# Optimization experiments

Hardware: AMD Instinct MI355X
Metric: run time of the kernel (lower is better)

## Reference

```python
import jax, jax.numpy as jnp
import numpy as np

VOCAB = 50257
K = 10  # accuracy_slack_size


def setup_inputs() -> dict:
    key = jax.random.key(0)
    k1, k2, k3, k4 = jax.random.split(key, 4)
    logits = jax.random.normal(k1, (4, 2048, 512), dtype=jnp.float32)
    target = jax.random.randint(k2, (4, 2048), 0, VOCAB, dtype=jnp.int64 if jax.config.jax_enable_x64 else jnp.int32)
    mask = jax.random.randint(k3, (4, 2048), 0, 2, dtype=jnp.int32)
    W = jax.random.normal(k4, (512, VOCAB), dtype=jnp.float32) * 0.02
    b = jnp.zeros((VOCAB,), dtype=jnp.float32)
    return {"logits": logits, "target": target, "mask": mask, "W": W, "b": b}


def reference(logits, target, mask, W, b):
    N = logits.shape[0] * logits.shape[1]
    x = logits.reshape(N, logits.shape[-1])            # [N, d]
    # sampled_softmax.log_prob: full log-softmax over vocab
    logp = jax.nn.log_softmax(x @ W + b, axis=-1)      # [N, V]
    _, words = jax.lax.top_k(logp, K)                  # [N, K] indices
    tgt = target.reshape(-1)                           # [N]
    msk = mask.reshape(-1).astype(jnp.float32)         # [N]
    # vectorized membership: is target among top-K predictions?
    hit = jnp.any(words == tgt[:, None], axis=1).astype(jnp.float32)
    counter = jnp.sum(hit * msk)
    all_counter = jnp.sum(msk)
    return jnp.array([counter / all_counter])
```

## Files before the change

### kernel.cpp

```cpp
#include <hip/hip_runtime.h>
#include <stdint.h>

#define V_VOCAB 50257
#define V_PAD   50304
#define NROWS   8192
#define DIM     512
#define KTOP    10
#define MARGIN  0.3f
#define ACH     8

typedef __attribute__((ext_vector_type(8))) short  short8;
typedef __attribute__((ext_vector_type(4))) float  f32x4;

struct Ctrl { int mc; int namb; int hits; int pad_; };

#define OFF_WT     0ULL
#define SZ_WT      51511296ULL
#define OFF_XC     (OFF_WT + SZ_WT)
#define SZ_XC      8388608ULL
#define OFF_BPAD   (OFF_XC + SZ_XC)
#define SZ_BPAD    (50304ULL*4)
#define OFF_ROWIDX (OFF_BPAD + SZ_BPAD)
#define OFF_THAT   (OFF_ROWIDX + 32768ULL)
#define OFF_COUNTS (OFF_THAT + 32768ULL)
#define OFF_AMB    (OFF_COUNTS + 32768ULL)
#define OFF_CTRL   (OFF_AMB + 32768ULL)
#define OFF_RK     (OFF_CTRL + 16ULL)
#define OFF_SST    (OFF_RK + 32768ULL)

#define GLOAD16(gp, lp) __builtin_amdgcn_global_load_lds( \
    (const __attribute__((address_space(1))) unsigned int*)(gp), \
    (__attribute__((address_space(3))) unsigned int*)(lp), 16, 0, 0)

__device__ __forceinline__ unsigned short f2bf(float f) {
  unsigned int u = __builtin_bit_cast(unsigned int, f);
  unsigned int r = (u + 0x7FFFu + ((u >> 16) & 1u)) >> 16;
  return (unsigned short)r;
}
__device__ __forceinline__ float bf2f(unsigned short h) {
  unsigned int u = ((unsigned int)h) << 16;
  return __builtin_bit_cast(float, u);
}

__global__ void k_prep(const int* __restrict__ mask, const float* __restrict__ b,
                       float* __restrict__ bpad, int* __restrict__ rowidx,
                       Ctrl* __restrict__ ctrl) {
  int i = blockIdx.x * 256 + threadIdx.x;
  if (i < V_PAD) bpad[i] = (i < V_VOCAB) ? b[i] : -1e30f;
  if (i < NROWS && mask[i] != 0) {
    int p = atomicAdd(&ctrl->mc, 1);
    rowidx[p] = i;
  }
}

__global__ void k_twt(const float* __restrict__ W, unsigned short* __restrict__ Wt) {
  __shared__ float lt[64][65];
  const int vbase = blockIdx.x * 64;
  const int kbase = blockIdx.y * 64;
  const int tid = threadIdx.x;
  const int krow = tid >> 6;
  const int col  = tid & 63;
  const int v    = vbase + col;
#pragma unroll
  for (int rr = 0; rr < 16; ++rr) {
    int kl = krow + rr * 4;
    float val = (v < V_VOCAB) ? W[(size_t)(kbase + kl) * V_VOCAB + v] : 0.0f;
    lt[kl][col] = val;
  }
  __syncthreads();
  const int vr = tid >> 3;
  const int kc = tid & 7;
#pragma unroll
  for (int p = 0; p < 2; ++p) {
    int vl = p * 32 + vr;
    short8 t;
#pragma unroll
    for (int j = 0; j < 8; ++j) t[j] = (short)f2bf(lt[kc * 8 + j][vl]);
    *(short8*)(Wt + (size_t)(vbase + vl) * DIM + kbase + kc * 8) = t;
  }
}

__global__ void k_xc(const float* __restrict__ x, const int* __restrict__ rowidx,
                     const Ctrl* __restrict__ ctrl, unsigned short* __restrict__ Xc) {
  const int wid = threadIdx.x >> 6, lane = threadIdx.x & 63;
  const int i = blockIdx.x * 4 + wid;
  const int mc = ctrl->mc;
  short8 t;
  if (i < mc) {
    const float* src = x + (size_t)rowidx[i] * DIM + lane * 8;
#pragma unroll
    for (int j = 0; j < 8; ++j) t[j] = (short)f2bf(src[j]);
  } else {
#pragma unroll
    for (int j = 0; j < 8; ++j) t[j] = 0;
  }
  *(short8*)(Xc + (size_t)i * DIM + lane * 8) = t;
}

__global__ void k_that(const unsigned short* __restrict__ Xc,
                       const unsigned short* __restrict__ Wt,
                       const float* __restrict__ bpad,
                       const int* __restrict__ rowidx, const int* __restrict__ target,
                       const Ctrl* __restrict__ ctrl, float* __restrict__ that) {
  const int wid = threadIdx.x >> 6, lane = threadIdx.x & 63;
  const int i = blockIdx.x * 4 + wid;
  const int mc = ctrl->mc;
  if (i >= mc) { if (lane == 0) that[i] = 1e30f; return; }
  const int tg = target[rowidx[i]];
  short8 xa = *(const short8*)(Xc + (size_t)i * DIM + lane * 8);
  short8 wa = *(const short8*)(Wt + (size_t)tg * DIM + lane * 8);
  float s = 0.f;
#pragma unroll
  for (int j = 0; j < 8; ++j)
    s += bf2f((unsigned short)xa[j]) * bf2f((unsigned short)wa[j]);
#pragma unroll
  for (int d = 1; d < 64; d <<= 1) s += __shfl_xor(s, d, 64);
  if (lane == 0) that[i] = s + bpad[tg];
}

__launch_bounds__(256, 2)
__global__ void k_count(const unsigned short* __restrict__ Xc,
                        const unsigned short* __restrict__ Wt,
                        const float* __restrict__ bpad, const float* __restrict__ that,
                        const Ctrl* __restrict__ ctrl, unsigned int* __restrict__ counts) {
  const int mc = ctrl->mc;
  const int mbase = blockIdx.y * 128;
  if (mbase >= mc) return;
  const int nbase = blockIdx.x * 128;

  __shared__ unsigned short sA[128 * 64];
  __shared__ unsigned short sB[128 * 64];
  char* sAc = (char*)sA;
  char* sBc = (char*)sB;

  const int tid = threadIdx.x;
  const int w = tid >> 6, lane = tid & 63;
  const int wm = (w >> 1) * 64, wn = (w & 1) * 64;

  const int srow = lane >> 3;
  const int s2   = (lane & 7) ^ srow;

  const char* Ab = (const char*)Xc + (size_t)mbase * 1024;
  const char* Bb = (const char*)Wt + (size_t)nbase * 1024;

  f32x4 acc[4][4];
#pragma unroll
  for (int a = 0; a < 4; ++a)
#pragma unroll
    for (int c = 0; c < 4; ++c) acc[a][c] = (f32x4)0.0f;

  for (int kt = 0; kt < 8; ++kt) {
    const int kk = kt * 128;
#pragma unroll
    for (int c = 0; c < 4; ++c) {
      const int row  = (w * 4 + c) * 8 + srow;
      const int loff = (w * 4 + c) * 1024 + lane * 16;
      GLOAD16(Ab + (size_t)row * 1024 + kk + s2 * 16, sAc + loff);
      GLOAD16(Bb + (size_t)row * 1024 + kk + s2 * 16, sBc + loff);
    }
    __syncthreads();
#pragma unroll
    for (int ks = 0; ks < 2; ++ks) {
      short8 af[4], bq[4];
#pragma unroll
      for (int mi = 0; mi < 4; ++mi) {
        const int r  = wm + mi * 16 + (lane & 15);
        const int sl = (ks * 4 + (lane >> 4)) ^ (r & 7);
        af[mi] = *(const short8*)(sAc + r * 128 + sl * 16);
      }
#pragma unroll
      for (int ni = 0; ni < 4; ++ni) {
        const int r  = wn + ni * 16 + (lane & 15);
        const int sl = (ks * 4 + (lane >> 4)) ^ (r & 7);
        bq[ni] = *(const short8*)(sBc + r * 128 + sl * 16);
      }
#pragma unroll
      for (int mi = 0; mi < 4; ++mi)
#pragma unroll
        for (int ni = 0; ni < 4; ++ni)
          acc[mi][ni] = __builtin_amdgcn_mfma_f32_16x16x32_bf16(
              af[mi], bq[ni], acc[mi][ni], 0, 0, 0);
    }
    __syncthreads();
  }

  float bv[4];
#pragma unroll
  for (int ni = 0; ni < 4; ++ni)
    bv[ni] = bpad[nbase + wn + ni * 16 + (lane & 15)];

#pragma unroll
  for (int mi = 0; mi < 4; ++mi) {
    unsigned int pc[4];
#pragma unroll
    for (int r = 0; r < 4; ++r) {
      const int m = mbase + wm + mi * 16 + (lane >> 4) * 4 + r;
      const float th  = that[m];
      const float tlo = th - MARGIN, thi = th + MARGIN;
      unsigned int p = 0;
#pragma unroll
      for (int ni = 0; ni < 4; ++ni) {
        const float s = acc[mi][ni][r] + bv[ni];
        p += (s > tlo) ? 1u : 0u;
        p += (s > thi) ? (1u << 16) : 0u;
      }
      pc[r] = p;
    }
#pragma unroll
    for (int r = 0; r < 4; ++r) {
      int p = (int)pc[r];
#pragma unroll
      for (int d = 1; d < 16; d <<= 1) p += __shfl_xor(p, d, 64);
      if ((lane & 15) == 0) {
        const int m = mbase + wm + mi * 16 + (lane >> 4) * 4 + r;
        atomicAdd(&counts[m], (unsigned int)p);
      }
    }
  }
}

__global__ void k_decide(const unsigned int* __restrict__ counts,
                         Ctrl* __restrict__ ctrl, int* __restrict__ amb) {
  const int i = blockIdx.x * 256 + threadIdx.x;
  if (i >= ctrl->mc) return;
  const unsigned int c = counts[i];
  const unsigned int lo = c & 0xFFFFu, hi = c >> 16;
  if (lo <= KTOP - 1) { atomicAdd(&ctrl->hits, 1); }
  else if (hi >= KTOP) {  }
  else { int p = atomicAdd(&ctrl->namb, 1); amb[p] = i; }
}

__global__ void k_fixt(const float* __restrict__ x, const float* __restrict__ W,
                       const float* __restrict__ b, const int* __restrict__ rowidx,
                       const int* __restrict__ target, const int* __restrict__ amb,
                       const Ctrl* __restrict__ ctrl, float* __restrict__ sst) {
  const int a = blockIdx.x * 64 + threadIdx.x;
  if (a >= ctrl->namb) return;
  const int n = rowidx[amb[a]];
  const int tg = target[n];
  float st = 0.f;
  for (int k = 0; k < DIM; ++k)
    st = fmaf(x[(size_t)n * DIM + k], W[(size_t)k * V_VOCAB + tg], st);
  sst[a] = st + b[tg];
}

__global__ void k_fixscan(const float* __restrict__ x, const float* __restrict__ W,
                          const float* __restrict__ b, const int* __restrict__ rowidx,
                          const int* __restrict__ target, const int* __restrict__ amb,
                          const float* __restrict__ sst, const Ctrl* __restrict__ ctrl,
                          int* __restrict__ rk) {
  __shared__ float sx[ACH][DIM];
  const int j = blockIdx.x * 256 + threadIdx.x;
  const int namb = ctrl->namb;
  const float bj = (j < V_VOCAB) ? b[j] : 0.f;
  for (int base = 0; base < namb; base += ACH) {
    __syncthreads();
    for (int t = threadIdx.x; t < ACH * DIM / 4; t += 256) {
      const int a  = t / (DIM / 4);
      const int kk = (t % (DIM / 4)) * 4;
      f32x4 v = (f32x4)0.f;
      if (base + a < namb) {
        const int n = rowidx[amb[base + a]];
        v = *(const f32x4*)(x + (size_t)n * DIM + kk);
      }
      *(f32x4*)(&sx[a][kk]) = v;
    }
    __syncthreads();
    if (j >= V_VOCAB) continue;
    float s[ACH];
#pragma unroll
    for (int a = 0; a < ACH; ++a) s[a] = 0.f;
    for (int k = 0; k < DIM; ++k) {
      const float wv = W[(size_t)k * V_VOCAB + j];
#pragma unroll
      for (int a = 0; a < ACH; ++a) s[a] = fmaf(sx[a][k], wv, s[a]);
    }
#pragma unroll
    for (int a = 0; a < ACH; ++a) {
      if (base + a < namb) {
        const int tg = target[rowidx[amb[base + a]]];
        const float sc = s[a] + bj;
        const float st = sst[base + a];
        if (sc > st || (sc == st && j < tg)) atomicAdd(&rk[base + a], 1);
      }
    }
  }
}

__global__ void k_fixdec(const int* __restrict__ rk, Ctrl* __restrict__ ctrl) {
  const int a = blockIdx.x * 256 + threadIdx.x;
  if (a < ctrl->namb && rk[a] <= KTOP - 1) atomicAdd(&ctrl->hits, 1);
}

__global__ void k_final(const Ctrl* __restrict__ ctrl, float* __restrict__ out) {
  out[0] = (float)ctrl->hits / (float)ctrl->mc;
}

extern "C" void kernel_launch(void* const* d_in, const int* in_sizes, int n_in,
                              void* d_out, int out_size, void* d_ws, size_t ws_size,
                              hipStream_t stream) {
  const float* x      = (const float*)d_in[0];
  const int*   target = (const int*)d_in[1];
  const int*   mask   = (const int*)d_in[2];
  const float* W      = (const float*)d_in[3];
  const float* b      = (const float*)d_in[4];
  float* out = (float*)d_out;

  char* ws = (char*)d_ws;
  unsigned short* Wt     = (unsigned short*)(ws + OFF_WT);
  unsigned short* Xc     = (unsigned short*)(ws + OFF_XC);
  float*          bpad   = (float*)(ws + OFF_BPAD);
  int*            rowidx = (int*)(ws + OFF_ROWIDX);
  float*          that   = (float*)(ws + OFF_THAT);
  unsigned int*   counts = (unsigned int*)(ws + OFF_COUNTS);
  int*            amb    = (int*)(ws + OFF_AMB);
  Ctrl*           ctrl   = (Ctrl*)(ws + OFF_CTRL);
  int*            rk     = (int*)(ws + OFF_RK);
  float*          sst    = (float*)(ws + OFF_SST);

  hipMemsetAsync(ws + OFF_COUNTS, 0, 32768 + 32768 + 16 + 32768, stream);

  k_prep   <<<197, 256, 0, stream>>>(mask, b, bpad, rowidx, ctrl);
  k_twt    <<<dim3(786, 8), 256, 0, stream>>>(W, Wt);
  k_xc     <<<2048, 256, 0, stream>>>(x, rowidx, ctrl, Xc);
  k_that   <<<2048, 256, 0, stream>>>(Xc, Wt, bpad, rowidx, target, ctrl, that);
  k_count  <<<dim3(393, 64), 256, 0, stream>>>(Xc, Wt, bpad, that, ctrl, counts);
  k_decide <<<32, 256, 0, stream>>>(counts, ctrl, amb);
  k_fixt   <<<128, 64, 0, stream>>>(x, W, b, rowidx, target, amb, ctrl, sst);
  k_fixscan<<<197, 256, 0, stream>>>(x, W, b, rowidx, target, amb, sst, ctrl, rk);
  k_fixdec <<<32, 256, 0, stream>>>(rk, ctrl);
  k_final  <<<1, 1, 0, stream>>>(ctrl, out);
}
```

Before: 544.1 us.

## Rewrite count GEMM as 256x256 tiles with double-buffered LDS pipeline

Replaces the 128x128 single-buffered k_count GEMM with a 256x256 tile using 512 threads and a 128KB double-buffered LDS ring. Global-to-LDS loads for the next K-slice are interleaved with MFMA work through explicit barriers and waitcnts, and MFMA sections run at raised priority. Workgroup IDs are remapped so consecutive blocks are spread across XCDs. Vocabulary padding grows to a multiple of 256 to fit the new tile. This adds register pressure from the 8x4 accumulators, and the large LDS footprint and hand-placed synchronisation could limit occupancy or be fragile.

Result: faster. 518.1 us (-4.8%).

```diff
diff --git a/kernel.cpp b/kernel.cpp
--- a/kernel.cpp
+++ b/kernel.cpp
@@ -2,7 +2,8 @@
 #include <stdint.h>
 
 #define V_VOCAB 50257
-#define V_PAD   50304
+#define V_PAD   50432
+#define NT_N    197
 #define NROWS   8192
 #define DIM     512
 #define KTOP    10
@@ -15,11 +16,11 @@
 struct Ctrl { int mc; int namb; int hits; int pad_; };
 
 #define OFF_WT     0ULL
-#define SZ_WT      51511296ULL
+#define SZ_WT      51642368ULL
 #define OFF_XC     (OFF_WT + SZ_WT)
 #define SZ_XC      8388608ULL
 #define OFF_BPAD   (OFF_XC + SZ_XC)
-#define SZ_BPAD    (50304ULL*4)
+#define SZ_BPAD    (50432ULL*4)
 #define OFF_ROWIDX (OFF_BPAD + SZ_BPAD)
 #define OFF_THAT   (OFF_ROWIDX + 32768ULL)
 #define OFF_COUNTS (OFF_THAT + 32768ULL)
@@ -31,6 +32,12 @@
 #define GLOAD16(gp, lp) __builtin_amdgcn_global_load_lds( \
     (const __attribute__((address_space(1))) unsigned int*)(gp), \
     (__attribute__((address_space(3))) unsigned int*)(lp), 16, 0, 0)
+
+#define SBAR()  do { asm volatile("" ::: "memory"); __builtin_amdgcn_s_barrier(); \
+                     asm volatile("" ::: "memory"); } while (0)
+#define LGKM0() asm volatile("s_waitcnt lgkmcnt(0)" ::: "memory")
+#define VM2()   asm volatile("s_waitcnt vmcnt(2)" ::: "memory")
+#define VM0()   asm volatile("s_waitcnt vmcnt(0)" ::: "memory")
 
 __device__ __forceinline__ unsigned short f2bf(float f) {
   unsigned int u = __builtin_bit_cast(unsigned int, f);
@@ -118,83 +125,126 @@
   if (lane == 0) that[i] = s + bpad[tg];
 }
 
-__launch_bounds__(256, 2)
+__launch_bounds__(512, 2)
 __global__ void k_count(const unsigned short* __restrict__ Xc,
                         const unsigned short* __restrict__ Wt,
                         const float* __restrict__ bpad, const float* __restrict__ that,
                         const Ctrl* __restrict__ ctrl, unsigned int* __restrict__ counts) {
   const int mc = ctrl->mc;
-  const int mbase = blockIdx.y * 128;
+  const int lin = blockIdx.y * NT_N + blockIdx.x;
+  const int wg  = (lin & 7) * 788 + (lin >> 3);
+  const int mt = wg & 31;
+  const int nt = wg >> 5;
+  const int mbase = mt * 256;
   if (mbase >= mc) return;
-  const int nbase = blockIdx.x * 128;
-
-  __shared__ unsigned short sA[128 * 64];
-  __shared__ unsigned short sB[128 * 64];
-  char* sAc = (char*)sA;
-  char* sBc = (char*)sB;
-
-  const int tid = threadIdx.x;
-  const int w = tid >> 6, lane = tid & 63;
-  const int wm = (w >> 1) * 64, wn = (w & 1) * 64;
-
-  const int srow = lane >> 3;
-  const int s2   = (lane & 7) ^ srow;
-
-  const char* Ab = (const char*)Xc + (size_t)mbase * 1024;
-  const char* Bb = (const char*)Wt + (size_t)nbase * 1024;
-
-  f32x4 acc[4][4];
-#pragma unroll
-  for (int a = 0; a < 4; ++a)
+  const int nbase = nt * 256;
+
+  __shared__ char lds[131072];
+
+  const int tid  = threadIdx.x;
+  const int lane = tid & 63;
+  const int w    = tid >> 6;
+  const int wr   = w >> 2;
+  const int wc   = w & 3;
+
+  const char* Ag = (const char*)Xc + (size_t)mbase * 1024;
+  const char* Bg = (const char*)Wt + (size_t)nbase * 1024;
+  const int s2 = (tid & 7) ^ ((tid >> 3) & 7);
+  const size_t gsrc_off = (size_t)(tid >> 3) * 1024 + (size_t)s2 * 16;
+  const int    ldst_off = (tid >> 3) * 128 + (tid & 7) * 16;
+
+#define STAGE_HALF(isA, q, h, ktb) do {                                        \
+    const char* _g = ((isA) ? Ag : Bg) + (size_t)(h) * 131072 + (size_t)(ktb) + gsrc_off; \
+    char* _l = lds + ((isA) ? 0 : 65536) + (q) * 32768 + (h) * 16384 + ldst_off; \
+    GLOAD16(_g, _l);                                                           \
+    GLOAD16(_g + 65536, _l + 8192);                                            \
+  } while (0)
+
+  const int fr = lane & 15;
+  const int fq = lane >> 4;
+  const int sl0 = (fq)     ^ (lane & 7);
+  const int sl1 = (4 + fq) ^ (lane & 7);
+
+#define LDA4(q, ks, mh) do {                                                   \
+    const char* _b = lds + (q) * 32768;                                        \
+    const int _sl = (ks) ? sl1 : sl0;                                          \
+    _Pragma("unroll") for (int _j = 0; _j < 4; ++_j) {                         \
+      const int _r = wr * 128 + (mh) * 64 + _j * 16 + fr;                      \
+      af[_j] = *(const short8*)(_b + _r * 128 + _sl * 16); }                   \
+  } while (0)
+#define LDB4(q, ks) do {                                                       \
+    const char* _b = lds + 65536 + (q) * 32768;                                \
+    const int _sl = (ks) ? sl1 : sl0;                                          \
+    _Pragma("unroll") for (int _j = 0; _j < 4; ++_j) {                         \
+      const int _r = wc * 64 + _j * 16 + fr;                                   \
+      bf[_j] = *(const short8*)(_b + _r * 128 + _sl * 16); }                   \
+  } while (0)
+#define MFMA16(mh) do {                                                        \
+    __builtin_amdgcn_s_setprio(1);                                             \
+    _Pragma("unroll") for (int _m = 0; _m < 4; ++_m)                           \
+    _Pragma("unroll") for (int _n = 0; _n < 4; ++_n)                           \
+      acc[(mh) * 4 + _m][_n] = __builtin_amdgcn_mfma_f32_16x16x32_bf16(        \
+          af[_m], bf[_n], acc[(mh) * 4 + _m][_n], 0, 0, 0);                    \
+    __builtin_amdgcn_s_setprio(0);                                             \
+  } while (0)
+
+  f32x4 acc[8][4];
+#pragma unroll
+  for (int a = 0; a < 8; ++a)
 #pragma unroll
     for (int c = 0; c < 4; ++c) acc[a][c] = (f32x4)0.0f;
 
-  for (int kt = 0; kt < 8; ++kt) {
-    const int kk = kt * 128;
-#pragma unroll
-    for (int c = 0; c < 4; ++c) {
-      const int row  = (w * 4 + c) * 8 + srow;
-      const int loff = (w * 4 + c) * 1024 + lane * 16;
-      GLOAD16(Ab + (size_t)row * 1024 + kk + s2 * 16, sAc + loff);
-      GLOAD16(Bb + (size_t)row * 1024 + kk + s2 * 16, sBc + loff);
-    }
-    __syncthreads();
-#pragma unroll
-    for (int ks = 0; ks < 2; ++ks) {
-      short8 af[4], bq[4];
-#pragma unroll
-      for (int mi = 0; mi < 4; ++mi) {
-        const int r  = wm + mi * 16 + (lane & 15);
-        const int sl = (ks * 4 + (lane >> 4)) ^ (r & 7);
-        af[mi] = *(const short8*)(sAc + r * 128 + sl * 16);
-      }
-#pragma unroll
-      for (int ni = 0; ni < 4; ++ni) {
-        const int r  = wn + ni * 16 + (lane & 15);
-        const int sl = (ks * 4 + (lane >> 4)) ^ (r & 7);
-        bq[ni] = *(const short8*)(sBc + r * 128 + sl * 16);
-      }
-#pragma unroll
-      for (int mi = 0; mi < 4; ++mi)
-#pragma unroll
-        for (int ni = 0; ni < 4; ++ni)
-          acc[mi][ni] = __builtin_amdgcn_mfma_f32_16x16x32_bf16(
-              af[mi], bq[ni], acc[mi][ni], 0, 0, 0);
-    }
-    __syncthreads();
-  }
+  short8 af[4], bf[4];
+
+  STAGE_HALF(0, 0, 0, 0);   STAGE_HALF(0, 0, 1, 0);
+  STAGE_HALF(1, 0, 0, 0);   STAGE_HALF(1, 0, 1, 0);
+  STAGE_HALF(0, 1, 0, 128);
+  VM2(); SBAR();
+
+#pragma unroll
+  for (int i = 0; i < 4; ++i) {
+    const int ktn  = (2 * i + 1) * 128;
+    const int ktp2 = (2 * i + 2 < 8 ? 2 * i + 2 : 0) * 128;
+    const int ktp3 = (2 * i + 3 < 8 ? 2 * i + 3 : 0) * 128;
+    LDB4(0, 0); LDA4(0, 0, 0);
+    STAGE_HALF(0, 1, 1, ktn);
+    SBAR(); LGKM0(); MFMA16(0); SBAR();
+    LDA4(0, 0, 1);
+    STAGE_HALF(1, 1, 0, ktn);
+    SBAR(); LGKM0(); MFMA16(1); SBAR();
+    LDB4(0, 1); LDA4(0, 1, 0);
+    STAGE_HALF(1, 1, 1, ktn);
+    SBAR(); LGKM0(); MFMA16(0); SBAR();
+    LDA4(0, 1, 1);
+    STAGE_HALF(0, 0, 0, ktp2);
+    SBAR(); LGKM0(); MFMA16(1);
+    VM2(); SBAR();
+    LDB4(1, 0); LDA4(1, 0, 0);
+    STAGE_HALF(0, 0, 1, ktp2);
+    SBAR(); LGKM0(); MFMA16(0); SBAR();
+    LDA4(1, 0, 1);
+    STAGE_HALF(1, 0, 0, ktp2);
+    SBAR(); LGKM0(); MFMA16(1); SBAR();
+    LDB4(1, 1); LDA4(1, 1, 0);
+    STAGE_HALF(1, 0, 1, ktp2);
+    SBAR(); LGKM0(); MFMA16(0); SBAR();
+    LDA4(1, 1, 1);
+    STAGE_HALF(0, 1, 0, ktp3);
+    SBAR(); LGKM0(); MFMA16(1);
+    VM2(); SBAR();
+  }
+  VM0();
 
   float bv[4];
 #pragma unroll
   for (int ni = 0; ni < 4; ++ni)
-    bv[ni] = bpad[nbase + wn + ni * 16 + (lane & 15)];
-
-#pragma unroll
-  for (int mi = 0; mi < 4; ++mi) {
-    unsigned int pc[4];
+    bv[ni] = bpad[nbase + wc * 64 + ni * 16 + fr];
+
+#pragma unroll
+  for (int mi = 0; mi < 8; ++mi) {
 #pragma unroll
     for (int r = 0; r < 4; ++r) {
-      const int m = mbase + wm + mi * 16 + (lane >> 4) * 4 + r;
+      const int m = mbase + wr * 128 + mi * 16 + fq * 4 + r;
       const float th  = that[m];
       const float tlo = th - MARGIN, thi = th + MARGIN;
       unsigned int p = 0;
@@ -204,19 +254,16 @@
         p += (s > tlo) ? 1u : 0u;
         p += (s > thi) ? (1u << 16) : 0u;
       }
-      pc[r] = p;
+      int pi = (int)p;
+#pragma unroll
+      for (int d = 1; d < 16; d <<= 1) pi += __shfl_xor(pi, d, 64);
+      if ((lane & 15) == 0) atomicAdd(&counts[m], (unsigned int)pi);
     }
-#pragma unroll
-    for (int r = 0; r < 4; ++r) {
-      int p = (int)pc[r];
-#pragma unroll
-      for (int d = 1; d < 16; d <<= 1) p += __shfl_xor(p, d, 64);
-      if ((lane & 15) == 0) {
-        const int m = mbase + wm + mi * 16 + (lane >> 4) * 4 + r;
-        atomicAdd(&counts[m], (unsigned int)p);
-      }
-    }
-  }
+  }
+#undef STAGE_HALF
+#undef LDA4
+#undef LDB4
+#undef MFMA16
 }
 
 __global__ void k_decide(const unsigned int* __restrict__ counts,
@@ -321,10 +368,10 @@
   hipMemsetAsync(ws + OFF_COUNTS, 0, 32768 + 32768 + 16 + 32768, stream);
 
   k_prep   <<<197, 256, 0, stream>>>(mask, b, bpad, rowidx, ctrl);
-  k_twt    <<<dim3(786, 8), 256, 0, stream>>>(W, Wt);
+  k_twt    <<<dim3(788, 8), 256, 0, stream>>>(W, Wt);
   k_xc     <<<2048, 256, 0, stream>>>(x, rowidx, ctrl, Xc);
   k_that   <<<2048, 256, 0, stream>>>(Xc, Wt, bpad, rowidx, target, ctrl, that);
-  k_count  <<<dim3(393, 64), 256, 0, stream>>>(Xc, Wt, bpad, that, ctrl, counts);
+  k_count  <<<dim3(NT_N, 32), 512, 0, stream>>>(Xc, Wt, bpad, that, ctrl, counts);
   k_decide <<<32, 256, 0, stream>>>(counts, ctrl, amb);
   k_fixt   <<<128, 64, 0, stream>>>(x, W, b, rowidx, target, amb, ctrl, sst);
   k_fixscan<<<197, 256, 0, stream>>>(x, W, b, rowidx, target, amb, sst, ctrl, rk);
```

## Keep full A tile in LDS and stream prepacked MFMA-layout W from global

Applied to the files above, without the earlier changes.

The count GEMM now loads the whole 128x512 bf16 activation tile into LDS once per block. W fragments are streamed straight from global memory into registers, with a three-stage rolling register prefetch. To make those direct loads match the MFMA B-operand layout, W is pre-transposed into a fragment-packed order by a new k_twt2 kernel, and k_that indexes that layout. Blocks grow to 512 threads covering 512 vocab columns, which removes the per-k-step barriers and LDS staging of W. The cost is about 128KB of LDS per block and a 128-accumulator register footprint, which limit occupancy, and W is re-read from L2 once per row block.

Measured after the change: 752.8 us. +38.4%, slower.

```diff
diff --git a/kernel.cpp b/kernel.cpp
--- a/kernel.cpp
+++ b/kernel.cpp
@@ -2,7 +2,8 @@
 #include <stdint.h>
 
 #define V_VOCAB 50257
-#define V_PAD   50304
+#define V_PAD2  50688
+#define NGB     99
 #define NROWS   8192
 #define DIM     512
 #define KTOP    10
@@ -14,12 +15,12 @@
 
 struct Ctrl { int mc; int namb; int hits; int pad_; };
 
-#define OFF_WT     0ULL
-#define SZ_WT      51511296ULL
-#define OFF_XC     (OFF_WT + SZ_WT)
+#define OFF_WT2    0ULL
+#define SZ_WT2     51904512ULL
+#define OFF_XC     (OFF_WT2 + SZ_WT2)
 #define SZ_XC      8388608ULL
 #define OFF_BPAD   (OFF_XC + SZ_XC)
-#define SZ_BPAD    (50304ULL*4)
+#define SZ_BPAD    (50688ULL*4)
 #define OFF_ROWIDX (OFF_BPAD + SZ_BPAD)
 #define OFF_THAT   (OFF_ROWIDX + 32768ULL)
 #define OFF_COUNTS (OFF_THAT + 32768ULL)
@@ -46,38 +47,26 @@
                        float* __restrict__ bpad, int* __restrict__ rowidx,
                        Ctrl* __restrict__ ctrl) {
   int i = blockIdx.x * 256 + threadIdx.x;
-  if (i < V_PAD) bpad[i] = (i < V_VOCAB) ? b[i] : -1e30f;
+  if (i < V_PAD2) bpad[i] = (i < V_VOCAB) ? b[i] : -1e30f;
   if (i < NROWS && mask[i] != 0) {
     int p = atomicAdd(&ctrl->mc, 1);
     rowidx[p] = i;
   }
 }
 
-__global__ void k_twt(const float* __restrict__ W, unsigned short* __restrict__ Wt) {
-  __shared__ float lt[64][65];
-  const int vbase = blockIdx.x * 64;
-  const int kbase = blockIdx.y * 64;
-  const int tid = threadIdx.x;
-  const int krow = tid >> 6;
-  const int col  = tid & 63;
-  const int v    = vbase + col;
-#pragma unroll
-  for (int rr = 0; rr < 16; ++rr) {
-    int kl = krow + rr * 4;
-    float val = (v < V_VOCAB) ? W[(size_t)(kbase + kl) * V_VOCAB + v] : 0.0f;
-    lt[kl][col] = val;
-  }
-  __syncthreads();
-  const int vr = tid >> 3;
-  const int kc = tid & 7;
-#pragma unroll
-  for (int p = 0; p < 2; ++p) {
-    int vl = p * 32 + vr;
-    short8 t;
-#pragma unroll
-    for (int j = 0; j < 8; ++j) t[j] = (short)f2bf(lt[kc * 8 + j][vl]);
-    *(short8*)(Wt + (size_t)(vbase + vl) * DIM + kbase + kc * 8) = t;
-  }
+__global__ void k_twt2(const float* __restrict__ W, unsigned short* __restrict__ Wt2) {
+  const int wv = threadIdx.x >> 6, lane = threadIdx.x & 63;
+  const int chunk = blockIdx.x * 4 + wv;
+  const int cb = chunk >> 4, ks = chunk & 15;
+  const int col = cb * 16 + (lane & 15);
+  const int kb  = ks * 32 + (lane >> 4) * 8;
+  short8 t;
+#pragma unroll
+  for (int jj = 0; jj < 8; ++jj) {
+    float v = (col < V_VOCAB) ? W[(size_t)(kb + jj) * V_VOCAB + col] : 0.0f;
+    t[jj] = (short)f2bf(v);
+  }
+  *(short8*)(Wt2 + (size_t)chunk * 512 + lane * 8) = t;
 }
 
 __global__ void k_xc(const float* __restrict__ x, const int* __restrict__ rowidx,
@@ -98,7 +87,7 @@
 }
 
 __global__ void k_that(const unsigned short* __restrict__ Xc,
-                       const unsigned short* __restrict__ Wt,
+                       const unsigned short* __restrict__ Wt2,
                        const float* __restrict__ bpad,
                        const int* __restrict__ rowidx, const int* __restrict__ target,
                        const Ctrl* __restrict__ ctrl, float* __restrict__ that) {
@@ -107,8 +96,10 @@
   const int mc = ctrl->mc;
   if (i >= mc) { if (lane == 0) that[i] = 1e30f; return; }
   const int tg = target[rowidx[i]];
+  const int cb = tg >> 4, cl = tg & 15;
+  const size_t u16 = ((size_t)(cb * 16 + (lane >> 2)) * 64 + (lane & 3) * 16 + cl);
   short8 xa = *(const short8*)(Xc + (size_t)i * DIM + lane * 8);
-  short8 wa = *(const short8*)(Wt + (size_t)tg * DIM + lane * 8);
+  short8 wa = *(const short8*)(Wt2 + u16 * 8);
   float s = 0.f;
 #pragma unroll
   for (int j = 0; j < 8; ++j)
@@ -118,103 +109,95 @@
   if (lane == 0) that[i] = s + bpad[tg];
 }
 
-__launch_bounds__(256, 2)
+__launch_bounds__(512, 2)
 __global__ void k_count(const unsigned short* __restrict__ Xc,
-                        const unsigned short* __restrict__ Wt,
+                        const unsigned short* __restrict__ Wt2,
                         const float* __restrict__ bpad, const float* __restrict__ that,
                         const Ctrl* __restrict__ ctrl, unsigned int* __restrict__ counts) {
   const int mc = ctrl->mc;
   const int mbase = blockIdx.y * 128;
   if (mbase >= mc) return;
-  const int nbase = blockIdx.x * 128;
-
-  __shared__ unsigned short sA[128 * 64];
-  __shared__ unsigned short sB[128 * 64];
-  char* sAc = (char*)sA;
-  char* sBc = (char*)sB;
-
-  const int tid = threadIdx.x;
-  const int w = tid >> 6, lane = tid & 63;
-  const int wm = (w >> 1) * 64, wn = (w & 1) * 64;
-
-  const int srow = lane >> 3;
-  const int s2   = (lane & 7) ^ srow;
-
-  const char* Ab = (const char*)Xc + (size_t)mbase * 1024;
-  const char* Bb = (const char*)Wt + (size_t)nbase * 1024;
-
-  f32x4 acc[4][4];
-#pragma unroll
-  for (int a = 0; a < 4; ++a)
+  const int nb = blockIdx.x;
+
+  __shared__ unsigned short sA[65536];
+  __shared__ float thr[128];
+
+  const int tid  = threadIdx.x;
+  const int lane = tid & 63;
+  const int w    = tid >> 6;
+
+  {
+    const int r0 = tid >> 6;
+    const int sl = (tid & 63) ^ (r0 & 7);
+    const char* src0 = (const char*)Xc + (((size_t)(mbase + r0)) << 10) + sl * 16;
+    char* dst0 = (char*)sA + tid * 16;
+#pragma unroll
+    for (int ch = 0; ch < 16; ++ch)
+      GLOAD16(src0 + (size_t)ch * 8192, dst0 + ch * 8192);
+  }
+  if (tid < 128) thr[tid] = that[mbase + tid];
+  __syncthreads();
+
+  const char* Bp = (const char*)Wt2 + ((size_t)(nb * 32 + w * 4) << 14);
+  const int fr = lane & 15;
+  const int fq = lane >> 4;
+
+  f32x4 acc[8][4];
+#pragma unroll
+  for (int a = 0; a < 8; ++a)
 #pragma unroll
     for (int c = 0; c < 4; ++c) acc[a][c] = (f32x4)0.0f;
 
-  for (int kt = 0; kt < 8; ++kt) {
-    const int kk = kt * 128;
-#pragma unroll
-    for (int c = 0; c < 4; ++c) {
-      const int row  = (w * 4 + c) * 8 + srow;
-      const int loff = (w * 4 + c) * 1024 + lane * 16;
-      GLOAD16(Ab + (size_t)row * 1024 + kk + s2 * 16, sAc + loff);
-      GLOAD16(Bb + (size_t)row * 1024 + kk + s2 * 16, sBc + loff);
-    }
-    __syncthreads();
-#pragma unroll
-    for (int ks = 0; ks < 2; ++ks) {
-      short8 af[4], bq[4];
-#pragma unroll
-      for (int mi = 0; mi < 4; ++mi) {
-        const int r  = wm + mi * 16 + (lane & 15);
-        const int sl = (ks * 4 + (lane >> 4)) ^ (r & 7);
-        af[mi] = *(const short8*)(sAc + r * 128 + sl * 16);
-      }
-#pragma unroll
-      for (int ni = 0; ni < 4; ++ni) {
-        const int r  = wn + ni * 16 + (lane & 15);
-        const int sl = (ks * 4 + (lane >> 4)) ^ (r & 7);
-        bq[ni] = *(const short8*)(sBc + r * 128 + sl * 16);
-      }
-#pragma unroll
-      for (int mi = 0; mi < 4; ++mi)
-#pragma unroll
-        for (int ni = 0; ni < 4; ++ni)
-          acc[mi][ni] = __builtin_amdgcn_mfma_f32_16x16x32_bf16(
-              af[mi], bq[ni], acc[mi][ni], 0, 0, 0);
-    }
-    __syncthreads();
+  short8 bq[3][4];
+#pragma unroll
+  for (int j = 0; j < 4; ++j) {
+    bq[0][j] = *(const short8*)(Bp + j * 16384 + 0 * 1024 + lane * 16);
+    bq[1][j] = *(const short8*)(Bp + j * 16384 + 1 * 1024 + lane * 16);
+  }
+
+#pragma unroll
+  for (int ks = 0; ks < 16; ++ks) {
+    if (ks + 2 < 16) {
+#pragma unroll
+      for (int j = 0; j < 4; ++j)
+        bq[(ks + 2) % 3][j] =
+            *(const short8*)(Bp + j * 16384 + (ks + 2) * 1024 + lane * 16);
+    }
+#pragma unroll
+    for (int mb = 0; mb < 8; ++mb) {
+      const int row = mb * 16 + fr;
+      const int phys = (ks * 4 + fq) ^ (fr & 7);
+      short8 a = *(const short8*)((const char*)sA + row * 1024 + phys * 16);
+#pragma unroll
+      for (int j = 0; j < 4; ++j)
+        acc[mb][j] = __builtin_amdgcn_mfma_f32_16x16x32_bf16(
+            a, bq[ks % 3][j], acc[mb][j], 0, 0, 0);
+    }
   }
 
   float bv[4];
 #pragma unroll
-  for (int ni = 0; ni < 4; ++ni)
-    bv[ni] = bpad[nbase + wn + ni * 16 + (lane & 15)];
-
-#pragma unroll
-  for (int mi = 0; mi < 4; ++mi) {
-    unsigned int pc[4];
+  for (int j = 0; j < 4; ++j)
+    bv[j] = bpad[nb * 512 + w * 64 + j * 16 + fr];
+
+#pragma unroll
+  for (int mb = 0; mb < 8; ++mb) {
 #pragma unroll
     for (int r = 0; r < 4; ++r) {
-      const int m = mbase + wm + mi * 16 + (lane >> 4) * 4 + r;
-      const float th  = that[m];
+      const float th  = thr[mb * 16 + fq * 4 + r];
       const float tlo = th - MARGIN, thi = th + MARGIN;
       unsigned int p = 0;
 #pragma unroll
-      for (int ni = 0; ni < 4; ++ni) {
-        const float s = acc[mi][ni][r] + bv[ni];
+      for (int j = 0; j < 4; ++j) {
+        const float s = acc[mb][j][r] + bv[j];
         p += (s > tlo) ? 1u : 0u;
         p += (s > thi) ? (1u << 16) : 0u;
       }
-      pc[r] = p;
-    }
-#pragma unroll
-    for (int r = 0; r < 4; ++r) {
-      int p = (int)pc[r];
-#pragma unroll
-      for (int d = 1; d < 16; d <<= 1) p += __shfl_xor(p, d, 64);
-      if ((lane & 15) == 0) {
-        const int m = mbase + wm + mi * 16 + (lane >> 4) * 4 + r;
-        atomicAdd(&counts[m], (unsigned int)p);
-      }
+      int pi = (int)p;
+#pragma unroll
+      for (int d = 1; d < 16; d <<= 1) pi += __shfl_xor(pi, d, 64);
+      if ((lane & 15) == 0)
+        atomicAdd(&counts[mbase + mb * 16 + fq * 4 + r], (unsigned int)pi);
     }
   }
 }
@@ -307,7 +290,7 @@
   float* out = (float*)d_out;
 
   char* ws = (char*)d_ws;
-  unsigned short* Wt     = (unsigned short*)(ws + OFF_WT);
+  unsigned short* Wt2    = (unsigned short*)(ws + OFF_WT2);
   unsigned short* Xc     = (unsigned short*)(ws + OFF_XC);
   float*          bpad   = (float*)(ws + OFF_BPAD);
   int*            rowidx = (int*)(ws + OFF_ROWIDX);
@@ -320,11 +303,11 @@
 
   hipMemsetAsync(ws + OFF_COUNTS, 0, 32768 + 32768 + 16 + 32768, stream);
 
-  k_prep   <<<197, 256, 0, stream>>>(mask, b, bpad, rowidx, ctrl);
-  k_twt    <<<dim3(786, 8), 256, 0, stream>>>(W, Wt);
+  k_prep   <<<198, 256, 0, stream>>>(mask, b, bpad, rowidx, ctrl);
+  k_twt2   <<<12672, 256, 0, stream>>>(W, Wt2);
   k_xc     <<<2048, 256, 0, stream>>>(x, rowidx, ctrl, Xc);
-  k_that   <<<2048, 256, 0, stream>>>(Xc, Wt, bpad, rowidx, target, ctrl, that);
-  k_count  <<<dim3(393, 64), 256, 0, stream>>>(Xc, Wt, bpad, that, ctrl, counts);
+  k_that   <<<2048, 256, 0, stream>>>(Xc, Wt2, bpad, rowidx, target, ctrl, that);
+  k_count  <<<dim3(NGB, 64), 512, 0, stream>>>(Xc, Wt2, bpad, that, ctrl, counts);
   k_decide <<<32, 256, 0, stream>>>(counts, ctrl, amb);
   k_fixt   <<<128, 64, 0, stream>>>(x, W, b, rowidx, target, amb, ctrl, sst);
   k_fixscan<<<197, 256, 0, stream>>>(x, W, b, rowidx, target, amb, sst, ctrl, rk);
```

## Triple-buffer the k_count GEMM with async LDS loads and 256x128 tiles

Applied to the files above, without the earlier changes.

Rewrites the main score-counting GEMM to use 512-thread blocks over 256x128 output tiles. Global-to-LDS loads now run through a three-stage buffer ring, with vmcnt waits and a single barrier per K-step, so loads overlap MFMA work instead of the old load/sync/compute/sync loop. MFMA priority is raised with setprio, and the vocab padding is widened to a multiple of 128 so the N tiling divides evenly. The 144 KB of LDS limits residency to one block per CU. The tail iterations issue redundant loads of the last K-tile to keep the wait counts uniform.

Measured after the change: 668.4 us. 22.9% more time.

```diff
diff --git a/kernel.cpp b/kernel.cpp
--- a/kernel.cpp
+++ b/kernel.cpp
@@ -2,7 +2,8 @@
 #include <stdint.h>
 
 #define V_VOCAB 50257
-#define V_PAD   50304
+#define V_PAD   50432
+#define NTB     394
 #define NROWS   8192
 #define DIM     512
 #define KTOP    10
@@ -15,11 +16,11 @@
 struct Ctrl { int mc; int namb; int hits; int pad_; };
 
 #define OFF_WT     0ULL
-#define SZ_WT      51511296ULL
+#define SZ_WT      51642368ULL
 #define OFF_XC     (OFF_WT + SZ_WT)
 #define SZ_XC      8388608ULL
 #define OFF_BPAD   (OFF_XC + SZ_XC)
-#define SZ_BPAD    (50304ULL*4)
+#define SZ_BPAD    (50432ULL*4)
 #define OFF_ROWIDX (OFF_BPAD + SZ_BPAD)
 #define OFF_THAT   (OFF_ROWIDX + 32768ULL)
 #define OFF_COUNTS (OFF_THAT + 32768ULL)
@@ -31,6 +32,11 @@
 #define GLOAD16(gp, lp) __builtin_amdgcn_global_load_lds( \
     (const __attribute__((address_space(1))) unsigned int*)(gp), \
     (__attribute__((address_space(3))) unsigned int*)(lp), 16, 0, 0)
+
+#define SBAR()  do { asm volatile("" ::: "memory"); __builtin_amdgcn_s_barrier(); \
+                     asm volatile("" ::: "memory"); } while (0)
+#define VM6()   asm volatile("s_waitcnt vmcnt(6)" ::: "memory")
+#define VM0()   asm volatile("s_waitcnt vmcnt(0)" ::: "memory")
 
 __device__ __forceinline__ unsigned short f2bf(float f) {
   unsigned int u = __builtin_bit_cast(unsigned int, f);
@@ -118,30 +124,44 @@
   if (lane == 0) that[i] = s + bpad[tg];
 }
 
-__launch_bounds__(256, 2)
+__launch_bounds__(512, 2)
 __global__ void k_count(const unsigned short* __restrict__ Xc,
                         const unsigned short* __restrict__ Wt,
                         const float* __restrict__ bpad, const float* __restrict__ that,
                         const Ctrl* __restrict__ ctrl, unsigned int* __restrict__ counts) {
   const int mc = ctrl->mc;
-  const int mbase = blockIdx.y * 128;
+  const int mbase = blockIdx.y * 256;
   if (mbase >= mc) return;
   const int nbase = blockIdx.x * 128;
 
-  __shared__ unsigned short sA[128 * 64];
-  __shared__ unsigned short sB[128 * 64];
-  char* sAc = (char*)sA;
-  char* sBc = (char*)sB;
-
-  const int tid = threadIdx.x;
-  const int w = tid >> 6, lane = tid & 63;
-  const int wm = (w >> 1) * 64, wn = (w & 1) * 64;
-
-  const int srow = lane >> 3;
-  const int s2   = (lane & 7) ^ srow;
-
-  const char* Ab = (const char*)Xc + (size_t)mbase * 1024;
-  const char* Bb = (const char*)Wt + (size_t)nbase * 1024;
+  __shared__ char lds[147456];
+
+  const int tid  = threadIdx.x;
+  const int lane = tid & 63;
+  const int w    = tid >> 6;
+  const int wr   = w >> 1;
+  const int wc   = w & 1;
+
+  const char* Ag = (const char*)Xc + (size_t)mbase * 1024;
+  const char* Bg = (const char*)Wt + (size_t)nbase * 1024;
+  const int sws  = ((tid & 7) ^ ((tid >> 3) & 7)) * 16;
+  const int r8   = tid >> 3;
+  const int dst0 = tid * 16;
+
+#define STAGE(q, kt) do {                                                      \
+    const size_t _kb = (size_t)(kt) * 128;                                     \
+    _Pragma("unroll") for (int _c = 0; _c < 4; ++_c)                           \
+      GLOAD16(Ag + (size_t)(_c * 64 + r8) * 1024 + _kb + sws,                  \
+              lds + (q) * 49152 + _c * 8192 + dst0);                           \
+    _Pragma("unroll") for (int _c = 0; _c < 2; ++_c)                           \
+      GLOAD16(Bg + (size_t)(_c * 64 + r8) * 1024 + _kb + sws,                  \
+              lds + (q) * 49152 + 32768 + _c * 8192 + dst0);                   \
+  } while (0)
+
+  const int fr = lane & 15;
+  const int fq = lane >> 4;
+  const int p0 = ((fq) ^ (fr & 7)) * 16;
+  const int p1 = ((4 + fq) ^ (fr & 7)) * 16;
 
   f32x4 acc[4][4];
 #pragma unroll
@@ -149,52 +169,47 @@
 #pragma unroll
     for (int c = 0; c < 4; ++c) acc[a][c] = (f32x4)0.0f;
 
-  for (int kt = 0; kt < 8; ++kt) {
-    const int kk = kt * 128;
-#pragma unroll
-    for (int c = 0; c < 4; ++c) {
-      const int row  = (w * 4 + c) * 8 + srow;
-      const int loff = (w * 4 + c) * 1024 + lane * 16;
-      GLOAD16(Ab + (size_t)row * 1024 + kk + s2 * 16, sAc + loff);
-      GLOAD16(Bb + (size_t)row * 1024 + kk + s2 * 16, sBc + loff);
-    }
-    __syncthreads();
-#pragma unroll
-    for (int ks = 0; ks < 2; ++ks) {
-      short8 af[4], bq[4];
-#pragma unroll
-      for (int mi = 0; mi < 4; ++mi) {
-        const int r  = wm + mi * 16 + (lane & 15);
-        const int sl = (ks * 4 + (lane >> 4)) ^ (r & 7);
-        af[mi] = *(const short8*)(sAc + r * 128 + sl * 16);
-      }
-#pragma unroll
-      for (int ni = 0; ni < 4; ++ni) {
-        const int r  = wn + ni * 16 + (lane & 15);
-        const int sl = (ks * 4 + (lane >> 4)) ^ (r & 7);
-        bq[ni] = *(const short8*)(sBc + r * 128 + sl * 16);
-      }
-#pragma unroll
-      for (int mi = 0; mi < 4; ++mi)
-#pragma unroll
-        for (int ni = 0; ni < 4; ++ni)
-          acc[mi][ni] = __builtin_amdgcn_mfma_f32_16x16x32_bf16(
-              af[mi], bq[ni], acc[mi][ni], 0, 0, 0);
-    }
-    __syncthreads();
-  }
+#define KTILE(q) do {                                                          \
+    const char* _ab = lds + (q) * 49152;                                       \
+    const char* _bb = _ab + 32768;                                             \
+    _Pragma("unroll") for (int _ks = 0; _ks < 2; ++_ks) {                      \
+      const int _p = _ks ? p1 : p0;                                            \
+      short8 a4[4], b4[4];                                                     \
+      _Pragma("unroll") for (int _i = 0; _i < 4; ++_i)                         \
+        a4[_i] = *(const short8*)(_ab + (wr * 64 + _i * 16 + fr) * 128 + _p);  \
+      _Pragma("unroll") for (int _i = 0; _i < 4; ++_i)                         \
+        b4[_i] = *(const short8*)(_bb + (wc * 64 + _i * 16 + fr) * 128 + _p);  \
+      __builtin_amdgcn_s_setprio(1);                                           \
+      _Pragma("unroll") for (int _m = 0; _m < 4; ++_m)                         \
+      _Pragma("unroll") for (int _n = 0; _n < 4; ++_n)                         \
+        acc[_m][_n] = __builtin_amdgcn_mfma_f32_16x16x32_bf16(                 \
+            a4[_m], b4[_n], acc[_m][_n], 0, 0, 0);                             \
+      __builtin_amdgcn_s_setprio(0);                                           \
+    }                                                                          \
+  } while (0)
+
+  STAGE(0, 0);
+  STAGE(1, 1);
+
+#pragma unroll
+  for (int t = 0; t < 8; ++t) {
+    VM6();
+    SBAR();
+    STAGE((t + 2) % 3, (t + 2 < 8) ? (t + 2) : 7);
+    KTILE(t % 3);
+  }
+  VM0();
 
   float bv[4];
 #pragma unroll
   for (int ni = 0; ni < 4; ++ni)
-    bv[ni] = bpad[nbase + wn + ni * 16 + (lane & 15)];
+    bv[ni] = bpad[nbase + wc * 64 + ni * 16 + fr];
 
 #pragma unroll
   for (int mi = 0; mi < 4; ++mi) {
-    unsigned int pc[4];
 #pragma unroll
     for (int r = 0; r < 4; ++r) {
-      const int m = mbase + wm + mi * 16 + (lane >> 4) * 4 + r;
+      const int m = mbase + wr * 64 + mi * 16 + fq * 4 + r;
       const float th  = that[m];
       const float tlo = th - MARGIN, thi = th + MARGIN;
       unsigned int p = 0;
@@ -204,19 +219,14 @@
         p += (s > tlo) ? 1u : 0u;
         p += (s > thi) ? (1u << 16) : 0u;
       }
-      pc[r] = p;
+      int pi = (int)p;
+#pragma unroll
+      for (int d = 1; d < 16; d <<= 1) pi += __shfl_xor(pi, d, 64);
+      if ((lane & 15) == 0) atomicAdd(&counts[m], (unsigned int)pi);
     }
-#pragma unroll
-    for (int r = 0; r < 4; ++r) {
-      int p = (int)pc[r];
-#pragma unroll
-      for (int d = 1; d < 16; d <<= 1) p += __shfl_xor(p, d, 64);
-      if ((lane & 15) == 0) {
-        const int m = mbase + wm + mi * 16 + (lane >> 4) * 4 + r;
-        atomicAdd(&counts[m], (unsigned int)p);
-      }
-    }
-  }
+  }
+#undef STAGE
+#undef KTILE
 }
 
 __global__ void k_decide(const unsigned int* __restrict__ counts,
@@ -321,10 +331,10 @@
   hipMemsetAsync(ws + OFF_COUNTS, 0, 32768 + 32768 + 16 + 32768, stream);
 
   k_prep   <<<197, 256, 0, stream>>>(mask, b, bpad, rowidx, ctrl);
-  k_twt    <<<dim3(786, 8), 256, 0, stream>>>(W, Wt);
+  k_twt    <<<dim3(788, 8), 256, 0, stream>>>(W, Wt);
   k_xc     <<<2048, 256, 0, stream>>>(x, rowidx, ctrl, Xc);
   k_that   <<<2048, 256, 0, stream>>>(Xc, Wt, bpad, rowidx, target, ctrl, that);
-  k_count  <<<dim3(393, 64), 256, 0, stream>>>(Xc, Wt, bpad, that, ctrl, counts);
+  k_count  <<<dim3(NTB, 32), 512, 0, stream>>>(Xc, Wt, bpad, that, ctrl, counts);
   k_decide <<<32, 256, 0, stream>>>(counts, ctrl, amb);
   k_fixt   <<<128, 64, 0, stream>>>(x, W, b, rowidx, target, amb, ctrl, sst);
   k_fixscan<<<197, 256, 0, stream>>>(x, W, b, rowidx, target, amb, sst, ctrl, rk);
```
